# Kernel optimization log

Measured on AMD Instinct MI355X. Metric: run time of the kernel, lower is better.

The kernel has to match this reference:

```python
import jax, jax.numpy as jnp
import numpy as np
import math

B, S, E, H, L = 16, 512, 256, 4, 2
D = E // H            # head size = 64
MAX_POS = 10
NUM_ITEMS = 50000


def setup_inputs() -> dict:
    key = jax.random.key(0)
    ks = jax.random.split(key, 16)
    s = 0.02
    item_inputs = jax.random.randint(ks[0], (B, S), 0, 2 * NUM_ITEMS + 1)
    item_ids = jax.random.randint(ks[1], (B, S), 0, NUM_ITEMS)
    input_embed = jax.random.normal(ks[2], (2 * NUM_ITEMS + 1, E), jnp.float32) * s
    input_embed = input_embed.at[0].set(0.0)  # padding_idx=0
    query_embed = jax.random.normal(ks[3], (NUM_ITEMS, E), jnp.float32) * s
    pos_key = jax.random.normal(ks[4], (MAX_POS, D), jnp.float32) * s
    pos_value = jax.random.normal(ks[5], (MAX_POS, D), jnp.float32) * s
    Wq = jax.random.normal(ks[6], (L, E, E), jnp.float32) * s
    bq = jnp.zeros((L, E), jnp.float32)
    Wk = jax.random.normal(ks[7], (L, E, E), jnp.float32) * s
    bk = jnp.zeros((L, E), jnp.float32)
    Wv = jax.random.normal(ks[8], (L, E, E), jnp.float32) * s
    bv = jnp.zeros((L, E), jnp.float32)
    Wo = jax.random.normal(ks[9], (L, E, E), jnp.float32) * s
    bo = jnp.zeros((L, E), jnp.float32)
    out_w = jax.random.normal(ks[10], (E, 1), jnp.float32) * s
    out_b = jnp.zeros((1,), jnp.float32)
    return dict(item_inputs=item_inputs, item_ids=item_ids,
                input_embed=input_embed, query_embed=query_embed,
                pos_key=pos_key, pos_value=pos_value,
                Wq=Wq, bq=bq, Wk=Wk, bk=bk, Wv=Wv, bv=bv, Wo=Wo, bo=bo,
                out_w=out_w, out_b=out_b)


def _heads(x, W, b):
    # [B,S,E] @ [E,E] -> [B,H,S,D]
    return (x @ W + b).reshape(B, S, H, D).transpose(0, 2, 1, 3)


def reference(item_inputs, item_ids, input_embed, query_embed, pos_key,
              pos_value, Wq, bq, Wk, bk, Wv, bv, Wo, bo, out_w, out_b):
    x = input_embed[item_inputs]          # [B,S,E]
    q_base = query_embed[item_ids]        # [B,S,E]

    i = jnp.arange(S)
    rel = jnp.clip(i[:, None] - i[None, :], 0, MAX_POS - 1)  # [S,S]
    pk = pos_key[rel]                     # [S,S,D]
    pv = pos_value[rel]                   # [S,S,D]
    causal = i[None, :] > i[:, None]      # future mask [S,S], True = masked
    scale = 1.0 / math.sqrt(D)

    out = x
    for l in range(L):
        qh = _heads(q_base, Wq[l], bq[l])
        kh = _heads(out, Wk[l], bk[l])
        vh = _heads(out, Wv[l], bv[l])
        # relative attention: scores = q.k^T + q.pos_key(i-j)
        scores = jnp.einsum('bhid,bhjd->bhij', qh, kh)
        scores = scores + jnp.einsum('bhid,ijd->bhij', qh, pk)
        scores = scores * scale
        scores = jnp.where(causal[None, None], -1e9, scores)
        p = jax.nn.softmax(scores, axis=-1)  # [B,H,S,S]
        # out_i = sum_j p_ij * (v_j + pos_value(i-j))
        attn = jnp.einsum('bhij,bhjd->bhid', p, vh) \
             + jnp.einsum('bhij,ijd->bhid', p, pv)
        merged = attn.transpose(0, 2, 1, 3).reshape(B, S, E)
        residual = merged @ Wo[l] + bo[l]
        out = out + jax.nn.relu(residual)
    return out @ out_w + out_b            # [B,S,1]
```

## Files before the change

kernel.cpp:

```cpp
#include <hip/hip_runtime.h>
#include <hip/hip_bf16.h>

#define B_ 16
#define S_ 512
#define E_ 256
#define H_ 4
#define D_ 64
#define L_ 2
#define MAXPOS 10

typedef __attribute__((ext_vector_type(8))) short bf16x8;
typedef __attribute__((ext_vector_type(4))) float f32x4;

static __device__ __forceinline__ short f2bf(float f) {
    __hip_bfloat16 h = __float2bfloat16(f);
    return __builtin_bit_cast(short, h);
}

static __device__ __forceinline__ void gload16(const void* g, void* l) {
    __builtin_amdgcn_global_load_lds(
        (const __attribute__((address_space(1))) void*)(g),
        (__attribute__((address_space(3))) void*)(l),
        16, 0, 0);
}

__global__ __launch_bounds__(256) void setup_kernel(
    const int* __restrict__ item_inputs, const int* __restrict__ item_ids,
    const float* __restrict__ input_embed, const float* __restrict__ query_embed,
    const float* __restrict__ Wq, const float* __restrict__ Wk,
    const float* __restrict__ Wv, const float* __restrict__ Wo,
    const float* __restrict__ pos_key, const float* __restrict__ out_b,
    float* __restrict__ outf, short* __restrict__ outb, short* __restrict__ qbb,
    short* __restrict__ Wt, short* __restrict__ pkb, float* __restrict__ y)
{
    const int tid = threadIdx.x;
    const int bx = blockIdx.x;
    if (bx < 8192) {
        const int row = bx;
        const int ii = item_inputs[row];
        const int qi = item_ids[row];
        const float xv = input_embed[(size_t)ii * E_ + tid];
        const float qv = query_embed[(size_t)qi * E_ + tid];
        const size_t idx = (size_t)row * E_ + tid;
        outf[idx] = xv;
        outb[idx] = f2bf(xv);
        qbb[idx] = f2bf(qv);
        return;
    }
    const int pb = bx - 8192;
    if (pb < 128) {
        __shared__ short tt[64 * 72];
        const int mId = pb >> 4;
        const int l = mId >> 2, which = mId & 3;
        const float* src = (which == 0 ? Wq : which == 1 ? Wk : which == 2 ? Wv : Wo)
                         + (size_t)l * E_ * E_;
        const int tr = (pb >> 2) & 3;
        const int tc = pb & 3;
        {
            const int kl = tid >> 2;
            const int nq = (tid & 3) * 16;
            const float* sp = src + (size_t)(tr * 64 + kl) * E_ + tc * 64 + nq;
            #pragma unroll
            for (int q = 0; q < 4; ++q) {
                const float4 v = reinterpret_cast<const float4*>(sp)[q];
                tt[(nq + q * 4 + 0) * 72 + kl] = f2bf(v.x);
                tt[(nq + q * 4 + 1) * 72 + kl] = f2bf(v.y);
                tt[(nq + q * 4 + 2) * 72 + kl] = f2bf(v.z);
                tt[(nq + q * 4 + 3) * 72 + kl] = f2bf(v.w);
            }
        }
        __syncthreads();
        {
            const int nl = tid >> 2;
            const int kq = (tid & 3) * 16;
            short* dst = Wt + (size_t)mId * 65536 + (size_t)(tc * 64 + nl) * E_ + tr * 64 + kq;
            *reinterpret_cast<bf16x8*>(&dst[0]) = *reinterpret_cast<const bf16x8*>(&tt[nl * 72 + kq]);
            *reinterpret_cast<bf16x8*>(&dst[8]) = *reinterpret_cast<const bf16x8*>(&tt[nl * 72 + kq + 8]);
        }
    } else if (pb == 128) {
        for (int idx = tid; idx < 16 * 64; idx += 256) {
            const int r = idx >> 6, d = idx & 63;
            pkb[idx] = (r < MAXPOS) ? f2bf(pos_key[r * 64 + d]) : (short)0;
        }
    } else {
        const float yb = out_b[0];
        for (int i = tid; i < 8192; i += 256) y[i] = yb;
    }
}

template<int MODE, int FINAL>
__global__ __launch_bounds__(256) void mfma_gemm_kernel(
    const short* __restrict__ Aq, const short* __restrict__ Akv,
    const short* __restrict__ Wt, const float* __restrict__ b0,
    const float* __restrict__ b1, const float* __restrict__ b2,
    short* __restrict__ C, float* __restrict__ outf, short* __restrict__ outb,
    const float* __restrict__ fw, float* __restrict__ y)
{
    __shared__ __align__(16) short As[64 * 256];
    __shared__ __align__(16) short Bs[64 * 256];
    const int bm = blockIdx.x, bn = blockIdx.y, z = blockIdx.z;
    const int tid = threadIdx.x;
    const int lane = tid & 63, w = tid >> 6;
    const int l15 = lane & 15, l4 = lane >> 4;

    const short* A;
    const short* W;
    const float* bias;
    if (MODE == 0) {
        A = (z == 0) ? Aq : Akv;
        W = Wt + (size_t)z * 65536;
        bias = (z == 0) ? b0 : (z == 1) ? b1 : b2;
    } else {
        A = Aq; W = Wt; bias = b0;
    }

    {
        const char* Ab = (const char*)A + (size_t)bm * 64 * 512;
        const char* Wb = (const char*)W + (size_t)bn * 64 * 512;
        #pragma unroll
        for (int c = 0; c < 8; ++c) {
            const int L = (w * 8 + c) * 1024 + lane * 16;
            const int src = L ^ (((L >> 9) & 7) << 4);
            gload16(Ab + src, (char*)As + (w * 8 + c) * 1024);
            gload16(Wb + src, (char*)Bs + (w * 8 + c) * 1024);
        }
    }
    __syncthreads();

    f32x4 acc[4];
    #pragma unroll
    for (int nf = 0; nf < 4; ++nf) acc[nf] = (f32x4){0.f, 0.f, 0.f, 0.f};

    const int sw = (l15 & 7) << 4;
    const int arow = w * 16 + l15;
    #pragma unroll
    for (int ks = 0; ks < 8; ++ks) {
        const int coff = (ks * 64 + l4 * 16) ^ sw;
        const bf16x8 af = *reinterpret_cast<const bf16x8*>(
            (const char*)As + arow * 512 + coff);
        #pragma unroll
        for (int nf = 0; nf < 4; ++nf) {
            const bf16x8 bfr = *reinterpret_cast<const bf16x8*>(
                (const char*)Bs + (nf * 16 + l15) * 512 + coff);
            acc[nf] = __builtin_amdgcn_mfma_f32_16x16x32_bf16(af, bfr, acc[nf], 0, 0, 0);
        }
    }

    short* Cz = (MODE == 0) ? C + (size_t)z * ((size_t)B_ * S_ * E_) : nullptr;
    float s[4] = {0.f, 0.f, 0.f, 0.f};
    #pragma unroll
    for (int nf = 0; nf < 4; ++nf) {
        const int col = bn * 64 + nf * 16 + l15;
        const float bb = bias[col];
        const float fwv = FINAL ? fw[col] : 0.0f;
        #pragma unroll
        for (int reg = 0; reg < 4; ++reg) {
            const int rowg = bm * 64 + w * 16 + l4 * 4 + reg;
            const float v = acc[nf][reg] + bb;
            const size_t idx = (size_t)rowg * E_ + col;
            if (MODE == 0) {
                Cz[idx] = f2bf(v);
            } else {
                const float o = outf[idx] + fmaxf(v, 0.0f);
                outf[idx] = o;
                outb[idx] = f2bf(o);
                if (FINAL) s[reg] += o * fwv;
            }
        }
    }
    if (FINAL) {
        #pragma unroll
        for (int m = 1; m < 16; m <<= 1) {
            #pragma unroll
            for (int reg = 0; reg < 4; ++reg) s[reg] += __shfl_xor(s[reg], m, 64);
        }
        if (l15 == 0) {
            #pragma unroll
            for (int reg = 0; reg < 4; ++reg)
                atomicAdd(&y[bm * 64 + w * 16 + l4 * 4 + reg], s[reg]);
        }
    }
}

__global__ __launch_bounds__(256) void attn_mfma_kernel(
    const short* __restrict__ Q, const short* __restrict__ K,
    const short* __restrict__ V, const short* __restrict__ pkb,
    const float* __restrict__ pos_value, short* __restrict__ merged)
{
    __shared__ __align__(16) short Qs[64 * 72];
    __shared__ __align__(16) short Ks[64 * 64];
    __shared__ __align__(16) short Vts[4656];
    __shared__ __align__(16) short Pl[4 * 16 * 72];
    __shared__ __align__(16) short Pk[16 * 72];
    __shared__ float pv_sh[MAXPOS * 64];
    __shared__ float qpk_sh[64 * 16];
    __shared__ float pdiag[64 * 9];

    const int bid = blockIdx.x;
    const int it = 7 - (bid & 7);
    const int h  = (bid >> 3) & 3;
    const int b  = bid >> 5;
    const int tid = threadIdx.x;
    const int lane = tid & 63;
    const int w = tid >> 6;
    const int l15 = lane & 15;
    const int l4  = lane >> 4;
    const int rloc  = l4 * 4;
    const int rbase = w * 16 + rloc;

    const size_t boff = (size_t)(b * S_) * E_ + h * D_;

    for (int idx = tid; idx < MAXPOS * 64; idx += 256) pv_sh[idx] = pos_value[idx];
    for (int idx = tid; idx < 64 * 9; idx += 256) pdiag[idx] = 0.0f;
    if (tid < 128) {
        const int r = tid >> 3, dq = (tid & 7) * 8;
        *reinterpret_cast<bf16x8*>(&Pk[r * 72 + dq]) =
            *reinterpret_cast<const bf16x8*>(&pkb[r * 64 + dq]);
    }
    {
        const int row = tid >> 2, dq = (tid & 3) * 16;
        const short* qp = &Q[boff + (size_t)(it * 64 + row) * E_ + dq];
        *reinterpret_cast<bf16x8*>(&Qs[row * 72 + dq]) =
            *reinterpret_cast<const bf16x8*>(qp);
        *reinterpret_cast<bf16x8*>(&Qs[row * 72 + dq + 8]) =
            *reinterpret_cast<const bf16x8*>(qp + 8);
    }
    __syncthreads();

    bf16x8 aq[2];
    #pragma unroll
    for (int ks = 0; ks < 2; ++ks)
        aq[ks] = *reinterpret_cast<const bf16x8*>(
            &Qs[(w * 16 + l15) * 72 + ks * 32 + 8 * l4]);

    f32x4 cq = (f32x4){0.f, 0.f, 0.f, 0.f};
    #pragma unroll
    for (int ks = 0; ks < 2; ++ks) {
        const bf16x8 bpk = *reinterpret_cast<const bf16x8*>(
            &Pk[l15 * 72 + ks * 32 + 8 * l4]);
        cq = __builtin_amdgcn_mfma_f32_16x16x32_bf16(aq[ks], bpk, cq, 0, 0, 0);
    }
    float q9[4];
    #pragma unroll
    for (int r = 0; r < 4; ++r) {
        qpk_sh[(rbase + r) * 16 + l15] = cq[r];
        q9[r] = __shfl(cq[r], l4 * 16 + 9, 64);
    }

    f32x4 accv[4];
    #pragma unroll
    for (int nf = 0; nf < 4; ++nf) accv[nf] = (f32x4){0.f, 0.f, 0.f, 0.f};
    float ls[4] = {0.f, 0.f, 0.f, 0.f};

    const int swl = (l15 & 7) << 4;

    for (int jt = 0; jt <= it; ++jt) {
        {
            const char* Kb = (const char*)(K + boff + (size_t)(jt * 64) * E_);
            #pragma unroll
            for (int c = 0; c < 2; ++c) {
                const int chunk = w * 2 + c;
                const int row = chunk * 8 + (lane >> 3);
                const int col = (lane & 7) * 16;
                const int src = row * 512 + (col ^ ((row & 7) << 4));
                gload16(Kb + src, (char*)Ks + chunk * 1024);
            }
            const int row = tid >> 2, dq = (tid & 3) * 16;
            const short* vp = &V[boff + (size_t)(jt * 64 + row) * E_ + dq];
            const bf16x8 v0 = *reinterpret_cast<const bf16x8*>(vp);
            const bf16x8 v1 = *reinterpret_cast<const bf16x8*>(vp + 8);
            const int skew = (tid & 3) * 32 + row * 2;
            #pragma unroll
            for (int e = 0; e < 8; ++e) {
                *(short*)((char*)Vts + (dq + e) * 144 + skew) = v0[e];
                *(short*)((char*)Vts + (dq + 8 + e) * 144 + skew) = v1[e];
            }
        }
        __syncthreads();

        const bool near = (jt >= it - 1);
        #pragma unroll
        for (int nf = 0; nf < 4; ++nf) {
            f32x4 c = (f32x4){0.f, 0.f, 0.f, 0.f};
            const int jrow = nf * 16 + l15;
            const bf16x8 bk0 = *reinterpret_cast<const bf16x8*>(
                (const char*)Ks + jrow * 128 + ((l4 * 16) ^ swl));
            const bf16x8 bk1 = *reinterpret_cast<const bf16x8*>(
                (const char*)Ks + jrow * 128 + ((64 + l4 * 16) ^ swl));
            c = __builtin_amdgcn_mfma_f32_16x16x32_bf16(aq[0], bk0, c, 0, 0, 0);
            c = __builtin_amdgcn_mfma_f32_16x16x32_bf16(aq[1], bk1, c, 0, 0, 0);
            const int j = jt * 64 + nf * 16 + l15;
            #pragma unroll
            for (int r = 0; r < 4; ++r) {
                float p;
                if (near) {
                    const int i = it * 64 + rbase + r;
                    const int rel = i - j;
                    if (rel < 0) p = 0.0f;
                    else {
                        const int rc = rel < 9 ? rel : 9;
                        p = __expf((c[r] + qpk_sh[(rbase + r) * 16 + rc]) * 0.125f);
                        if (rel < 9) pdiag[(rbase + r) * 9 + rel] = p;
                    }
                } else {
                    p = __expf((c[r] + q9[r]) * 0.125f);
                }
                ls[r] += p;
                Pl[w * 1152 + (rloc + r) * 72 + nf * 16 + l15] = f2bf(p);
            }
        }
        #pragma unroll
        for (int ks = 0; ks < 2; ++ks) {
            const bf16x8 pa = *reinterpret_cast<const bf16x8*>(
                &Pl[w * 1152 + l15 * 72 + ks * 32 + 8 * l4]);
            #pragma unroll
            for (int nf = 0; nf < 4; ++nf) {
                const int d = nf * 16 + l15;
                const bf16x8 bv = *reinterpret_cast<const bf16x8*>(
                    (const char*)Vts + d * 144 + nf * 32 + ks * 64 + l4 * 16);
                accv[nf] = __builtin_amdgcn_mfma_f32_16x16x32_bf16(pa, bv, accv[nf], 0, 0, 0);
            }
        }
        __syncthreads();
    }

    #pragma unroll
    for (int m = 1; m < 16; m <<= 1) {
        #pragma unroll
        for (int r = 0; r < 4; ++r) ls[r] += __shfl_xor(ls[r], m, 64);
    }

    #pragma unroll
    for (int r = 0; r < 4; ++r) {
        const int rowl = rbase + r;
        const float inv = 1.0f / ls[r];
        #pragma unroll
        for (int nf = 0; nf < 4; ++nf) {
            const int col = nf * 16 + l15;
            const float pv9 = pv_sh[9 * 64 + col];
            float extra = ls[r] * pv9;
            #pragma unroll
            for (int rr = 0; rr < 9; ++rr)
                extra += pdiag[rowl * 9 + rr] * (pv_sh[rr * 64 + col] - pv9);
            merged[boff + (size_t)(it * 64 + rowl) * E_ + col] =
                f2bf((accv[nf][r] + extra) * inv);
        }
    }
}

extern "C" void kernel_launch(void* const* d_in, const int* in_sizes, int n_in,
                              void* d_out, int out_size, void* d_ws, size_t ws_size,
                              hipStream_t stream) {
    const int*   item_inputs = (const int*)d_in[0];
    const int*   item_ids    = (const int*)d_in[1];
    const float* input_embed = (const float*)d_in[2];
    const float* query_embed = (const float*)d_in[3];
    const float* pos_key     = (const float*)d_in[4];
    const float* pos_value   = (const float*)d_in[5];
    const float* Wq = (const float*)d_in[6];
    const float* bq = (const float*)d_in[7];
    const float* Wk = (const float*)d_in[8];
    const float* bk = (const float*)d_in[9];
    const float* Wv = (const float*)d_in[10];
    const float* bv = (const float*)d_in[11];
    const float* Wo = (const float*)d_in[12];
    const float* bo = (const float*)d_in[13];
    const float* out_w = (const float*)d_in[14];
    const float* out_b = (const float*)d_in[15];
    float* y = (float*)d_out;

    char* w8 = (char*)d_ws;
    float* outf = (float*)(w8);
    short* outb = (short*)(w8 + ((size_t)8  << 20));
    short* qbb  = (short*)(w8 + ((size_t)12 << 20));
    short* Qb   = (short*)(w8 + ((size_t)16 << 20));
    short* mgb  = (short*)(w8 + ((size_t)28 << 20));
    short* Wt   = (short*)(w8 + ((size_t)32 << 20));
    short* pkb  = (short*)(w8 + ((size_t)33 << 20));

    const size_t HS = (size_t)B_ * S_ * E_;

    setup_kernel<<<8192 + 130, 256, 0, stream>>>(
        item_inputs, item_ids, input_embed, query_embed,
        Wq, Wk, Wv, Wo, pos_key, out_b, outf, outb, qbb, Wt, pkb, y);

    for (int l = 0; l < L_; ++l) {
        mfma_gemm_kernel<0, 0><<<dim3(128, 4, 3), 256, 0, stream>>>(
            qbb, outb, Wt + (size_t)l * 262144,
            bq + l * E_, bk + l * E_, bv + l * E_, Qb, nullptr, nullptr,
            nullptr, nullptr);
        attn_mfma_kernel<<<B_ * H_ * (S_ / 64), 256, 0, stream>>>(
            Qb, Qb + HS, Qb + 2 * HS, pkb, pos_value, mgb);
        if (l == L_ - 1) {
            mfma_gemm_kernel<1, 1><<<dim3(128, 4, 1), 256, 0, stream>>>(
                mgb, nullptr, Wt + (size_t)l * 262144 + 3 * 65536,
                bo + l * E_, nullptr, nullptr, nullptr, outf, outb, out_w, y);
        } else {
            mfma_gemm_kernel<1, 0><<<dim3(128, 4, 1), 256, 0, stream>>>(
                mgb, nullptr, Wt + (size_t)l * 262144 + 3 * 65536,
                bo + l * E_, nullptr, nullptr, nullptr, outf, outb, nullptr, nullptr);
        }
    }
}
```

Before: 100.7 us.

## Fuse O-projection with next-layer QKV, pair attention tiles, vectorize setup gather

Restructures the pipeline into fewer launches. The layer-0 output projection, its residual, and the layer-1 QKV projection are fused into one kernel that double-buffers the weight tiles. Attention blocks now process a long and a short causal query tile together for load balance, with 256 blocks instead of 512. pos_key conversion moves into the attention kernel, and the embedding gather is vectorized over 16 rows per block. The final kernel skips writing back the residual stream. The cost is that the fused kernel runs only 128 blocks, which lowers parallelism.

```diff
diff --git a/kernel.cpp b/kernel.cpp
--- a/kernel.cpp
+++ b/kernel.cpp
@@ -8,6 +8,7 @@
 #define D_ 64
 #define L_ 2
 #define MAXPOS 10
+#define HS_ ((size_t)B_ * S_ * E_)
 
 typedef __attribute__((ext_vector_type(8))) short bf16x8;
 typedef __attribute__((ext_vector_type(4))) float f32x4;
@@ -24,30 +25,69 @@
         16, 0, 0);
 }
 
+static __device__ __forceinline__ void stage_tile(const char* gbase, char* lds,
+                                                  int w, int lane) {
+    #pragma unroll
+    for (int c = 0; c < 8; ++c) {
+        const int L = (w * 8 + c) * 1024 + lane * 16;
+        const int src = L ^ (((L >> 9) & 7) << 4);
+        gload16(gbase + src, lds + (w * 8 + c) * 1024);
+    }
+}
+
+static __device__ __forceinline__ void gemm_compute(const short* As, const short* Bs,
+                                                    f32x4* acc, int w, int l15, int l4) {
+    const int sw = (l15 & 7) << 4;
+    const int arow = w * 16 + l15;
+    #pragma unroll
+    for (int nf = 0; nf < 4; ++nf) acc[nf] = (f32x4){0.f, 0.f, 0.f, 0.f};
+    #pragma unroll
+    for (int ks = 0; ks < 8; ++ks) {
+        const int coff = (ks * 64 + l4 * 16) ^ sw;
+        const bf16x8 af = *reinterpret_cast<const bf16x8*>((const char*)As + arow * 512 + coff);
+        #pragma unroll
+        for (int nf = 0; nf < 4; ++nf) {
+            const bf16x8 bfr = *reinterpret_cast<const bf16x8*>(
+                (const char*)Bs + (nf * 16 + l15) * 512 + coff);
+            acc[nf] = __builtin_amdgcn_mfma_f32_16x16x32_bf16(af, bfr, acc[nf], 0, 0, 0);
+        }
+    }
+}
+
 __global__ __launch_bounds__(256) void setup_kernel(
     const int* __restrict__ item_inputs, const int* __restrict__ item_ids,
     const float* __restrict__ input_embed, const float* __restrict__ query_embed,
     const float* __restrict__ Wq, const float* __restrict__ Wk,
     const float* __restrict__ Wv, const float* __restrict__ Wo,
-    const float* __restrict__ pos_key, const float* __restrict__ out_b,
+    const float* __restrict__ out_b,
     float* __restrict__ outf, short* __restrict__ outb, short* __restrict__ qbb,
-    short* __restrict__ Wt, short* __restrict__ pkb, float* __restrict__ y)
+    short* __restrict__ Wt, float* __restrict__ y)
 {
     const int tid = threadIdx.x;
     const int bx = blockIdx.x;
-    if (bx < 8192) {
-        const int row = bx;
+    if (bx < 512) {
+        const int rr = tid >> 4, c0 = (tid & 15) * 16;
+        const int row = bx * 16 + rr;
         const int ii = item_inputs[row];
         const int qi = item_ids[row];
-        const float xv = input_embed[(size_t)ii * E_ + tid];
-        const float qv = query_embed[(size_t)qi * E_ + tid];
-        const size_t idx = (size_t)row * E_ + tid;
-        outf[idx] = xv;
-        outb[idx] = f2bf(xv);
-        qbb[idx] = f2bf(qv);
+        const float* xs = input_embed + (size_t)ii * E_ + c0;
+        const float* qs = query_embed + (size_t)qi * E_ + c0;
+        float* of = outf + (size_t)row * E_ + c0;
+        short* ob = outb + (size_t)row * E_ + c0;
+        short* qb = qbb + (size_t)row * E_ + c0;
+        #pragma unroll
+        for (int q = 0; q < 4; ++q) {
+            const float4 xv = reinterpret_cast<const float4*>(xs)[q];
+            const float4 qv = reinterpret_cast<const float4*>(qs)[q];
+            reinterpret_cast<float4*>(of)[q] = xv;
+            short4 xb = { f2bf(xv.x), f2bf(xv.y), f2bf(xv.z), f2bf(xv.w) };
+            short4 qb4 = { f2bf(qv.x), f2bf(qv.y), f2bf(qv.z), f2bf(qv.w) };
+            reinterpret_cast<short4*>(ob)[q] = xb;
+            reinterpret_cast<short4*>(qb)[q] = qb4;
+        }
         return;
     }
-    const int pb = bx - 8192;
+    const int pb = bx - 512;
     if (pb < 128) {
         __shared__ short tt[64 * 72];
         const int mId = pb >> 4;
@@ -78,23 +118,16 @@
             *reinterpret_cast<bf16x8*>(&dst[8]) = *reinterpret_cast<const bf16x8*>(&tt[nl * 72 + kq + 8]);
         }
     } else if (pb == 128) {
-        for (int idx = tid; idx < 16 * 64; idx += 256) {
-            const int r = idx >> 6, d = idx & 63;
-            pkb[idx] = (r < MAXPOS) ? f2bf(pos_key[r * 64 + d]) : (short)0;
-        }
-    } else {
         const float yb = out_b[0];
         for (int i = tid; i < 8192; i += 256) y[i] = yb;
     }
 }
 
-template<int MODE, int FINAL>
-__global__ __launch_bounds__(256) void mfma_gemm_kernel(
-    const short* __restrict__ Aq, const short* __restrict__ Akv,
-    const short* __restrict__ Wt, const float* __restrict__ b0,
-    const float* __restrict__ b1, const float* __restrict__ b2,
-    short* __restrict__ C, float* __restrict__ outf, short* __restrict__ outb,
-    const float* __restrict__ fw, float* __restrict__ y)
+__global__ __launch_bounds__(256) void qkv0_kernel(
+    const short* __restrict__ qbb, const short* __restrict__ outb,
+    const short* __restrict__ Wt, const float* __restrict__ bq,
+    const float* __restrict__ bk, const float* __restrict__ bv,
+    short* __restrict__ Qb)
 {
     __shared__ __align__(16) short As[64 * 256];
     __shared__ __align__(16) short Bs[64 * 256];
@@ -103,88 +136,33 @@
     const int lane = tid & 63, w = tid >> 6;
     const int l15 = lane & 15, l4 = lane >> 4;
 
-    const short* A;
-    const short* W;
-    const float* bias;
-    if (MODE == 0) {
-        A = (z == 0) ? Aq : Akv;
-        W = Wt + (size_t)z * 65536;
-        bias = (z == 0) ? b0 : (z == 1) ? b1 : b2;
-    } else {
-        A = Aq; W = Wt; bias = b0;
-    }
-
-    {
-        const char* Ab = (const char*)A + (size_t)bm * 64 * 512;
-        const char* Wb = (const char*)W + (size_t)bn * 64 * 512;
-        #pragma unroll
-        for (int c = 0; c < 8; ++c) {
-            const int L = (w * 8 + c) * 1024 + lane * 16;
-            const int src = L ^ (((L >> 9) & 7) << 4);
-            gload16(Ab + src, (char*)As + (w * 8 + c) * 1024);
-            gload16(Wb + src, (char*)Bs + (w * 8 + c) * 1024);
-        }
-    }
+    const short* A = (z == 0) ? qbb : outb;
+    const short* W = Wt + (size_t)z * 65536;
+    const float* bias = (z == 0) ? bq : (z == 1) ? bk : bv;
+
+    stage_tile((const char*)A + (size_t)bm * 32768, (char*)As, w, lane);
+    stage_tile((const char*)W + (size_t)bn * 32768, (char*)Bs, w, lane);
     __syncthreads();
 
     f32x4 acc[4];
-    #pragma unroll
-    for (int nf = 0; nf < 4; ++nf) acc[nf] = (f32x4){0.f, 0.f, 0.f, 0.f};
-
-    const int sw = (l15 & 7) << 4;
-    const int arow = w * 16 + l15;
-    #pragma unroll
-    for (int ks = 0; ks < 8; ++ks) {
-        const int coff = (ks * 64 + l4 * 16) ^ sw;
-        const bf16x8 af = *reinterpret_cast<const bf16x8*>(
-            (const char*)As + arow * 512 + coff);
-        #pragma unroll
-        for (int nf = 0; nf < 4; ++nf) {
-            const bf16x8 bfr = *reinterpret_cast<const bf16x8*>(
-                (const char*)Bs + (nf * 16 + l15) * 512 + coff);
-            acc[nf] = __builtin_amdgcn_mfma_f32_16x16x32_bf16(af, bfr, acc[nf], 0, 0, 0);
-        }
-    }
-
-    short* Cz = (MODE == 0) ? C + (size_t)z * ((size_t)B_ * S_ * E_) : nullptr;
-    float s[4] = {0.f, 0.f, 0.f, 0.f};
+    gemm_compute(As, Bs, acc, w, l15, l4);
+
+    short* Cz = Qb + (size_t)z * HS_;
     #pragma unroll
     for (int nf = 0; nf < 4; ++nf) {
         const int col = bn * 64 + nf * 16 + l15;
         const float bb = bias[col];
-        const float fwv = FINAL ? fw[col] : 0.0f;
         #pragma unroll
         for (int reg = 0; reg < 4; ++reg) {
             const int rowg = bm * 64 + w * 16 + l4 * 4 + reg;
-            const float v = acc[nf][reg] + bb;
-            const size_t idx = (size_t)rowg * E_ + col;
-            if (MODE == 0) {
-                Cz[idx] = f2bf(v);
-            } else {
-                const float o = outf[idx] + fmaxf(v, 0.0f);
-                outf[idx] = o;
-                outb[idx] = f2bf(o);
-                if (FINAL) s[reg] += o * fwv;
-            }
-        }
-    }
-    if (FINAL) {
-        #pragma unroll
-        for (int m = 1; m < 16; m <<= 1) {
-            #pragma unroll
-            for (int reg = 0; reg < 4; ++reg) s[reg] += __shfl_xor(s[reg], m, 64);
-        }
-        if (l15 == 0) {
-            #pragma unroll
-            for (int reg = 0; reg < 4; ++reg)
-                atomicAdd(&y[bm * 64 + w * 16 + l4 * 4 + reg], s[reg]);
-        }
-    }
-}
-
-__global__ __launch_bounds__(256) void attn_mfma_kernel(
+            Cz[(size_t)rowg * E_ + col] = f2bf(acc[nf][reg] + bb);
+        }
+    }
+}
+
+__global__ __launch_bounds__(256) void attn2_kernel(
     const short* __restrict__ Q, const short* __restrict__ K,
-    const short* __restrict__ V, const short* __restrict__ pkb,
+    const short* __restrict__ V, const float* __restrict__ pos_key,
     const float* __restrict__ pos_value, short* __restrict__ merged)
 {
     __shared__ __align__(16) short Qs[64 * 72];
@@ -197,9 +175,9 @@
     __shared__ float pdiag[64 * 9];
 
     const int bid = blockIdx.x;
-    const int it = 7 - (bid & 7);
-    const int h  = (bid >> 3) & 3;
-    const int b  = bid >> 5;
+    const int a = bid & 3;
+    const int h = (bid >> 2) & 3;
+    const int b = bid >> 4;
     const int tid = threadIdx.x;
     const int lane = tid & 63;
     const int w = tid >> 6;
@@ -207,144 +185,256 @@
     const int l4  = lane >> 4;
     const int rloc  = l4 * 4;
     const int rbase = w * 16 + rloc;
+    const int swl = (l15 & 7) << 4;
 
     const size_t boff = (size_t)(b * S_) * E_ + h * D_;
 
     for (int idx = tid; idx < MAXPOS * 64; idx += 256) pv_sh[idx] = pos_value[idx];
-    for (int idx = tid; idx < 64 * 9; idx += 256) pdiag[idx] = 0.0f;
-    if (tid < 128) {
-        const int r = tid >> 3, dq = (tid & 7) * 8;
-        *reinterpret_cast<bf16x8*>(&Pk[r * 72 + dq]) =
-            *reinterpret_cast<const bf16x8*>(&pkb[r * 64 + dq]);
-    }
-    {
-        const int row = tid >> 2, dq = (tid & 3) * 16;
-        const short* qp = &Q[boff + (size_t)(it * 64 + row) * E_ + dq];
-        *reinterpret_cast<bf16x8*>(&Qs[row * 72 + dq]) =
-            *reinterpret_cast<const bf16x8*>(qp);
-        *reinterpret_cast<bf16x8*>(&Qs[row * 72 + dq + 8]) =
-            *reinterpret_cast<const bf16x8*>(qp + 8);
-    }
+    for (int idx = tid; idx < 16 * 64; idx += 256) {
+        const int r = idx >> 6, d = idx & 63;
+        Pk[r * 72 + d] = (r < MAXPOS) ? f2bf(pos_key[r * 64 + d]) : (short)0;
+    }
+
+    for (int pass = 0; pass < 2; ++pass) {
+        const int it = pass ? a : 7 - a;
+        if (pass) __syncthreads();
+        for (int idx = tid; idx < 64 * 9; idx += 256) pdiag[idx] = 0.0f;
+        {
+            const int row = tid >> 2, dq = (tid & 3) * 16;
+            const short* qp = &Q[boff + (size_t)(it * 64 + row) * E_ + dq];
+            *reinterpret_cast<bf16x8*>(&Qs[row * 72 + dq]) = *reinterpret_cast<const bf16x8*>(qp);
+            *reinterpret_cast<bf16x8*>(&Qs[row * 72 + dq + 8]) = *reinterpret_cast<const bf16x8*>(qp + 8);
+        }
+        __syncthreads();
+
+        bf16x8 aq[2];
+        #pragma unroll
+        for (int ks = 0; ks < 2; ++ks)
+            aq[ks] = *reinterpret_cast<const bf16x8*>(&Qs[(w * 16 + l15) * 72 + ks * 32 + 8 * l4]);
+
+        f32x4 cq = (f32x4){0.f, 0.f, 0.f, 0.f};
+        #pragma unroll
+        for (int ks = 0; ks < 2; ++ks) {
+            const bf16x8 bpk = *reinterpret_cast<const bf16x8*>(&Pk[l15 * 72 + ks * 32 + 8 * l4]);
+            cq = __builtin_amdgcn_mfma_f32_16x16x32_bf16(aq[ks], bpk, cq, 0, 0, 0);
+        }
+        float q9[4];
+        #pragma unroll
+        for (int r = 0; r < 4; ++r) {
+            qpk_sh[(rbase + r) * 16 + l15] = cq[r] * 0.125f;
+            q9[r] = __shfl(cq[r], l4 * 16 + 9, 64) * 0.125f;
+        }
+
+        f32x4 accv[4];
+        #pragma unroll
+        for (int nf = 0; nf < 4; ++nf) accv[nf] = (f32x4){0.f, 0.f, 0.f, 0.f};
+        float ls[4] = {0.f, 0.f, 0.f, 0.f};
+
+        for (int jt = 0; jt <= it; ++jt) {
+            {
+                const char* Kb = (const char*)(K + boff + (size_t)(jt * 64) * E_);
+                #pragma unroll
+                for (int c = 0; c < 2; ++c) {
+                    const int chunk = w * 2 + c;
+                    const int row = chunk * 8 + (lane >> 3);
+                    const int col = (lane & 7) * 16;
+                    const int src = row * 512 + (col ^ ((row & 7) << 4));
+                    gload16(Kb + src, (char*)Ks + chunk * 1024);
+                }
+                const int row = tid >> 2, dq = (tid & 3) * 16;
+                const short* vp = &V[boff + (size_t)(jt * 64 + row) * E_ + dq];
+                const bf16x8 v0 = *reinterpret_cast<const bf16x8*>(vp);
+                const bf16x8 v1 = *reinterpret_cast<const bf16x8*>(vp + 8);
+                const int skew = (tid & 3) * 32 + row * 2;
+                #pragma unroll
+                for (int e = 0; e < 8; ++e) {
+                    *(short*)((char*)Vts + (dq + e) * 144 + skew) = v0[e];
+                    *(short*)((char*)Vts + (dq + 8 + e) * 144 + skew) = v1[e];
+                }
+            }
+            __syncthreads();
+
+            const bool near = (jt >= it - 1);
+            #pragma unroll
+            for (int nf = 0; nf < 4; ++nf) {
+                f32x4 c = (f32x4){0.f, 0.f, 0.f, 0.f};
+                const int jrow = nf * 16 + l15;
+                const bf16x8 bk0 = *reinterpret_cast<const bf16x8*>(
+                    (const char*)Ks + jrow * 128 + ((l4 * 16) ^ swl));
+                const bf16x8 bk1 = *reinterpret_cast<const bf16x8*>(
+                    (const char*)Ks + jrow * 128 + ((64 + l4 * 16) ^ swl));
+                c = __builtin_amdgcn_mfma_f32_16x16x32_bf16(aq[0], bk0, c, 0, 0, 0);
+                c = __builtin_amdgcn_mfma_f32_16x16x32_bf16(aq[1], bk1, c, 0, 0, 0);
+                const int j = jt * 64 + nf * 16 + l15;
+                #pragma unroll
+                for (int r = 0; r < 4; ++r) {
+                    float pp;
+                    if (near) {
+                        const int i = it * 64 + rbase + r;
+                        const int rel = i - j;
+                        if (rel < 0) pp = 0.0f;
+                        else {
+                            const int rc = rel < 9 ? rel : 9;
+                            pp = __expf(fmaf(c[r], 0.125f, qpk_sh[(rbase + r) * 16 + rc]));
+                            if (rel < 9) pdiag[(rbase + r) * 9 + rel] = pp;
+                        }
+                    } else {
+                        pp = __expf(fmaf(c[r], 0.125f, q9[r]));
+                    }
+                    ls[r] += pp;
+                    Pl[w * 1152 + (rloc + r) * 72 + nf * 16 + l15] = f2bf(pp);
+                }
+            }
+            #pragma unroll
+            for (int ks = 0; ks < 2; ++ks) {
+                const bf16x8 pa = *reinterpret_cast<const bf16x8*>(
+                    &Pl[w * 1152 + l15 * 72 + ks * 32 + 8 * l4]);
+                #pragma unroll
+                for (int nf = 0; nf < 4; ++nf) {
+                    const int d = nf * 16 + l15;
+                    const bf16x8 bv = *reinterpret_cast<const bf16x8*>(
+                        (const char*)Vts + d * 144 + nf * 32 + ks * 64 + l4 * 16);
+                    accv[nf] = __builtin_amdgcn_mfma_f32_16x16x32_bf16(pa, bv, accv[nf], 0, 0, 0);
+                }
+            }
+            __syncthreads();
+        }
+
+        #pragma unroll
+        for (int m = 1; m < 16; m <<= 1) {
+            #pragma unroll
+            for (int r = 0; r < 4; ++r) ls[r] += __shfl_xor(ls[r], m, 64);
+        }
+
+        #pragma unroll
+        for (int r = 0; r < 4; ++r) {
+            const int rowl = rbase + r;
+            const float inv = 1.0f / ls[r];
+            #pragma unroll
+            for (int nf = 0; nf < 4; ++nf) {
+                const int col = nf * 16 + l15;
+                const float pv9 = pv_sh[9 * 64 + col];
+                float extra = ls[r] * pv9;
+                #pragma unroll
+                for (int rr = 0; rr < 9; ++rr)
+                    extra += pdiag[rowl * 9 + rr] * (pv_sh[rr * 64 + col] - pv9);
+                merged[boff + (size_t)(it * 64 + rowl) * E_ + col] =
+                    f2bf((accv[nf][r] + extra) * inv);
+            }
+        }
+    }
+}
+
+__global__ __launch_bounds__(256) void oqkv_kernel(
+    const short* __restrict__ qbb, const short* __restrict__ mgb,
+    const short* __restrict__ Wt, const float* __restrict__ bo0,
+    const float* __restrict__ bq1, const float* __restrict__ bk1,
+    const float* __restrict__ bv1, float* __restrict__ outf,
+    short* __restrict__ Qb)
+{
+    __shared__ __align__(16) short Qs2[64 * 256];
+    __shared__ __align__(16) short Xs[64 * 256];
+    __shared__ __align__(16) short Bs[2][64 * 256];
+    const int bm = blockIdx.x;
+    const int tid = threadIdx.x, lane = tid & 63, w = tid >> 6;
+    const int l15 = lane & 15, l4 = lane >> 4;
+
+    stage_tile((const char*)qbb + (size_t)bm * 32768, (char*)Qs2, w, lane);
+    stage_tile((const char*)mgb + (size_t)bm * 32768, (char*)Xs, w, lane);
+    stage_tile((const char*)(Wt + 3 * 65536), (char*)Bs[0], w, lane);
+
+    f32x4 accO[4][4];
+    for (int t = 0; t < 16; ++t) {
+        __syncthreads();
+        if (t + 1 < 16) {
+            const int tn = t + 1;
+            const size_t off = (tn < 4)
+                ? ((size_t)3 * 65536 + (size_t)tn * 16384)
+                : ((size_t)(4 + ((tn - 4) >> 2)) * 65536 + (size_t)((tn - 4) & 3) * 16384);
+            stage_tile((const char*)(Wt + off), (char*)Bs[tn & 1], w, lane);
+        }
+        if (t < 4) {
+            gemm_compute(Xs, Bs[t & 1], accO[t], w, l15, l4);
+            if (t == 3) {
+                __syncthreads();
+                #pragma unroll
+                for (int bn = 0; bn < 4; ++bn) {
+                    #pragma unroll
+                    for (int nf = 0; nf < 4; ++nf) {
+                        const int col = bn * 64 + nf * 16 + l15;
+                        const float bb = bo0[col];
+                        #pragma unroll
+                        for (int reg = 0; reg < 4; ++reg) {
+                            const int row = w * 16 + l4 * 4 + reg;
+                            const size_t gidx = (size_t)(bm * 64 + row) * E_ + col;
+                            const float o = outf[gidx] + fmaxf(accO[bn][nf][reg] + bb, 0.0f);
+                            outf[gidx] = o;
+                            *(short*)((char*)Xs + row * 512 + ((2 * col) ^ ((row & 7) << 4))) = f2bf(o);
+                        }
+                    }
+                }
+            }
+        } else {
+            const int z = (t - 4) >> 2, bn = (t - 4) & 3;
+            f32x4 acc[4];
+            gemm_compute((z == 0) ? Qs2 : Xs, Bs[t & 1], acc, w, l15, l4);
+            const float* bias = (z == 0) ? bq1 : (z == 1) ? bk1 : bv1;
+            short* Cz = Qb + (size_t)z * HS_;
+            #pragma unroll
+            for (int nf = 0; nf < 4; ++nf) {
+                const int col = bn * 64 + nf * 16 + l15;
+                const float bb = bias[col];
+                #pragma unroll
+                for (int reg = 0; reg < 4; ++reg) {
+                    const int rowg = bm * 64 + w * 16 + l4 * 4 + reg;
+                    Cz[(size_t)rowg * E_ + col] = f2bf(acc[nf][reg] + bb);
+                }
+            }
+        }
+    }
+}
+
+__global__ __launch_bounds__(256) void o1final_kernel(
+    const short* __restrict__ mgb, const short* __restrict__ Wt7,
+    const float* __restrict__ bo1, const float* __restrict__ outf,
+    const float* __restrict__ fw, float* __restrict__ y)
+{
+    __shared__ __align__(16) short As[64 * 256];
+    __shared__ __align__(16) short Bs[64 * 256];
+    const int bm = blockIdx.x, bn = blockIdx.y;
+    const int tid = threadIdx.x;
+    const int lane = tid & 63, w = tid >> 6;
+    const int l15 = lane & 15, l4 = lane >> 4;
+
+    stage_tile((const char*)mgb + (size_t)bm * 32768, (char*)As, w, lane);
+    stage_tile((const char*)(Wt7 + (size_t)bn * 16384), (char*)Bs, w, lane);
     __syncthreads();
 
-    bf16x8 aq[2];
-    #pragma unroll
-    for (int ks = 0; ks < 2; ++ks)
-        aq[ks] = *reinterpret_cast<const bf16x8*>(
-            &Qs[(w * 16 + l15) * 72 + ks * 32 + 8 * l4]);
-
-    f32x4 cq = (f32x4){0.f, 0.f, 0.f, 0.f};
-    #pragma unroll
-    for (int ks = 0; ks < 2; ++ks) {
-        const bf16x8 bpk = *reinterpret_cast<const bf16x8*>(
-            &Pk[l15 * 72 + ks * 32 + 8 * l4]);
-        cq = __builtin_amdgcn_mfma_f32_16x16x32_bf16(aq[ks], bpk, cq, 0, 0, 0);
-    }
-    float q9[4];
-    #pragma unroll
-    for (int r = 0; r < 4; ++r) {
-        qpk_sh[(rbase + r) * 16 + l15] = cq[r];
-        q9[r] = __shfl(cq[r], l4 * 16 + 9, 64);
-    }
-
-    f32x4 accv[4];
-    #pragma unroll
-    for (int nf = 0; nf < 4; ++nf) accv[nf] = (f32x4){0.f, 0.f, 0.f, 0.f};
-    float ls[4] = {0.f, 0.f, 0.f, 0.f};
-
-    const int swl = (l15 & 7) << 4;
-
-    for (int jt = 0; jt <= it; ++jt) {
-        {
-            const char* Kb = (const char*)(K + boff + (size_t)(jt * 64) * E_);
-            #pragma unroll
-            for (int c = 0; c < 2; ++c) {
-                const int chunk = w * 2 + c;
-                const int row = chunk * 8 + (lane >> 3);
-                const int col = (lane & 7) * 16;
-                const int src = row * 512 + (col ^ ((row & 7) << 4));
-                gload16(Kb + src, (char*)Ks + chunk * 1024);
-            }
-            const int row = tid >> 2, dq = (tid & 3) * 16;
-            const short* vp = &V[boff + (size_t)(jt * 64 + row) * E_ + dq];
-            const bf16x8 v0 = *reinterpret_cast<const bf16x8*>(vp);
-            const bf16x8 v1 = *reinterpret_cast<const bf16x8*>(vp + 8);
-            const int skew = (tid & 3) * 32 + row * 2;
-            #pragma unroll
-            for (int e = 0; e < 8; ++e) {
-                *(short*)((char*)Vts + (dq + e) * 144 + skew) = v0[e];
-                *(short*)((char*)Vts + (dq + 8 + e) * 144 + skew) = v1[e];
-            }
-        }
-        __syncthreads();
-
-        const bool near = (jt >= it - 1);
-        #pragma unroll
-        for (int nf = 0; nf < 4; ++nf) {
-            f32x4 c = (f32x4){0.f, 0.f, 0.f, 0.f};
-            const int jrow = nf * 16 + l15;
-            const bf16x8 bk0 = *reinterpret_cast<const bf16x8*>(
-                (const char*)Ks + jrow * 128 + ((l4 * 16) ^ swl));
-            const bf16x8 bk1 = *reinterpret_cast<const bf16x8*>(
-                (const char*)Ks + jrow * 128 + ((64 + l4 * 16) ^ swl));
-            c = __builtin_amdgcn_mfma_f32_16x16x32_bf16(aq[0], bk0, c, 0, 0, 0);
-            c = __builtin_amdgcn_mfma_f32_16x16x32_bf16(aq[1], bk1, c, 0, 0, 0);
-            const int j = jt * 64 + nf * 16 + l15;
-            #pragma unroll
-            for (int r = 0; r < 4; ++r) {
-                float p;
-                if (near) {
-                    const int i = it * 64 + rbase + r;
-                    const int rel = i - j;
-                    if (rel < 0) p = 0.0f;
-                    else {
-                        const int rc = rel < 9 ? rel : 9;
-                        p = __expf((c[r] + qpk_sh[(rbase + r) * 16 + rc]) * 0.125f);
-                        if (rel < 9) pdiag[(rbase + r) * 9 + rel] = p;
-                    }
-                } else {
-                    p = __expf((c[r] + q9[r]) * 0.125f);
-                }
-                ls[r] += p;
-                Pl[w * 1152 + (rloc + r) * 72 + nf * 16 + l15] = f2bf(p);
-            }
-        }
-        #pragma unroll
-        for (int ks = 0; ks < 2; ++ks) {
-            const bf16x8 pa = *reinterpret_cast<const bf16x8*>(
-                &Pl[w * 1152 + l15 * 72 + ks * 32 + 8 * l4]);
-            #pragma unroll
-            for (int nf = 0; nf < 4; ++nf) {
-                const int d = nf * 16 + l15;
-                const bf16x8 bv = *reinterpret_cast<const bf16x8*>(
-                    (const char*)Vts + d * 144 + nf * 32 + ks * 64 + l4 * 16);
-                accv[nf] = __builtin_amdgcn_mfma_f32_16x16x32_bf16(pa, bv, accv[nf], 0, 0, 0);
-            }
-        }
-        __syncthreads();
-    }
-
+    f32x4 acc[4];
+    gemm_compute(As, Bs, acc, w, l15, l4);
+
+    float s[4] = {0.f, 0.f, 0.f, 0.f};
+    #pragma unroll
+    for (int nf = 0; nf < 4; ++nf) {
+        const int col = bn * 64 + nf * 16 + l15;
+        const float bb = bo1[col];
+        const float fwv = fw[col];
+        #pragma unroll
+        for (int reg = 0; reg < 4; ++reg) {
+            const int rowg = bm * 64 + w * 16 + l4 * 4 + reg;
+            const float o = outf[(size_t)rowg * E_ + col] + fmaxf(acc[nf][reg] + bb, 0.0f);
+            s[reg] += o * fwv;
+        }
+    }
     #pragma unroll
     for (int m = 1; m < 16; m <<= 1) {
         #pragma unroll
-        for (int r = 0; r < 4; ++r) ls[r] += __shfl_xor(ls[r], m, 64);
-    }
-
-    #pragma unroll
-    for (int r = 0; r < 4; ++r) {
-        const int rowl = rbase + r;
-        const float inv = 1.0f / ls[r];
-        #pragma unroll
-        for (int nf = 0; nf < 4; ++nf) {
-            const int col = nf * 16 + l15;
-            const float pv9 = pv_sh[9 * 64 + col];
-            float extra = ls[r] * pv9;
-            #pragma unroll
-            for (int rr = 0; rr < 9; ++rr)
-                extra += pdiag[rowl * 9 + rr] * (pv_sh[rr * 64 + col] - pv9);
-            merged[boff + (size_t)(it * 64 + rowl) * E_ + col] =
-                f2bf((accv[nf][r] + extra) * inv);
-        }
+        for (int reg = 0; reg < 4; ++reg) s[reg] += __shfl_xor(s[reg], m, 64);
+    }
+    if (l15 == 0) {
+        #pragma unroll
+        for (int reg = 0; reg < 4; ++reg)
+            atomicAdd(&y[bm * 64 + w * 16 + l4 * 4 + reg], s[reg]);
     }
 }
 
@@ -376,29 +466,23 @@
     short* Qb   = (short*)(w8 + ((size_t)16 << 20));
     short* mgb  = (short*)(w8 + ((size_t)28 << 20));
     short* Wt   = (short*)(w8 + ((size_t)32 << 20));
-    short* pkb  = (short*)(w8 + ((size_t)33 << 20));
-
-    const size_t HS = (size_t)B_ * S_ * E_;
-
-    setup_kernel<<<8192 + 130, 256, 0, stream>>>(
+
+    setup_kernel<<<641, 256, 0, stream>>>(
         item_inputs, item_ids, input_embed, query_embed,
-        Wq, Wk, Wv, Wo, pos_key, out_b, outf, outb, qbb, Wt, pkb, y);
-
-    for (int l = 0; l < L_; ++l) {
-        mfma_gemm_kernel<0, 0><<<dim3(128, 4, 3), 256, 0, stream>>>(
-            qbb, outb, Wt + (size_t)l * 262144,
-            bq + l * E_, bk + l * E_, bv + l * E_, Qb, nullptr, nullptr,
-            nullptr, nullptr);
-        attn_mfma_kernel<<<B_ * H_ * (S_ / 64), 256, 0, stream>>>(
-            Qb, Qb + HS, Qb + 2 * HS, pkb, pos_value, mgb);
-        if (l == L_ - 1) {
-            mfma_gemm_kernel<1, 1><<<dim3(128, 4, 1), 256, 0, stream>>>(
-                mgb, nullptr, Wt + (size_t)l * 262144 + 3 * 65536,
-                bo + l * E_, nullptr, nullptr, nullptr, outf, outb, out_w, y);
-        } else {
-            mfma_gemm_kernel<1, 0><<<dim3(128, 4, 1), 256, 0, stream>>>(
-                mgb, nullptr, Wt + (size_t)l * 262144 + 3 * 65536,
-                bo + l * E_, nullptr, nullptr, nullptr, outf, outb, nullptr, nullptr);
-        }
-    }
-}
+        Wq, Wk, Wv, Wo, out_b, outf, outb, qbb, Wt, y);
+
+    qkv0_kernel<<<dim3(128, 4, 3), 256, 0, stream>>>(
+        qbb, outb, Wt, bq, bk, bv, Qb);
+
+    attn2_kernel<<<256, 256, 0, stream>>>(
+        Qb, Qb + HS_, Qb + 2 * HS_, pos_key, pos_value, mgb);
+
+    oqkv_kernel<<<128, 256, 0, stream>>>(
+        qbb, mgb, Wt, bo, bq + E_, bk + E_, bv + E_, outf, Qb);
+
+    attn2_kernel<<<256, 256, 0, stream>>>(
+        Qb, Qb + HS_, Qb + 2 * HS_, pos_key, pos_value, mgb);
+
+    o1final_kernel<<<dim3(128, 4), 256, 0, stream>>>(
+        mgb, Wt + (size_t)7 * 65536, bo + E_, outf, out_w, y);
+}
```

New measurement: 127.6 us. +26.7%, slower.
